# Kernel tuning notes

Hardware: AMD Instinct MI355X
Metric: run time of the kernel (lower is better)

Reference implementation:

```python
import jax, jax.numpy as jnp
import numpy as np

EPS = 1e-5


def _whiten(feature):
    # ZCA whitening per sample (WCT): f_w = U diag(s^-1/2) U^T (f - mean)
    b, c, h, w = feature.shape
    f = feature.reshape(b, c, h * w)
    mean = f.mean(axis=-1, keepdims=True)
    f = f - mean
    cov = jnp.einsum('bcx,bdx->bcd', f, f) / (h * w - 1)
    s, u = jnp.linalg.eigh(cov)
    s = jnp.maximum(s, EPS)
    out = jnp.einsum('bcd,bd,bed,bex->bcx', u, s ** -0.5, u, f)
    return out.reshape(b, c, h, w)


def _color(feature, target):
    # ZCA coloring: f_c = Ut diag(st^1/2) Ut^T (f - mean_f) + mean_t
    b, c, h, w = feature.shape
    f = feature.reshape(b, c, h * w)
    f = f - f.mean(axis=-1, keepdims=True)
    t = target.reshape(b, c, -1)
    tmean = t.mean(axis=-1, keepdims=True)
    tc = t - tmean
    cov = jnp.einsum('bcx,bdx->bcd', tc, tc) / (tc.shape[-1] - 1)
    s, u = jnp.linalg.eigh(cov)
    s = jnp.maximum(s, EPS)
    out = jnp.einsum('bcd,bd,bed,bex->bcx', u, s ** 0.5, u, f) + tmean
    return out.reshape(b, c, h, w)


def _patches(f, p):
    # [b,c,h,w] -> [b,c,h,w,p*p], same ordering as torch unfold(2,p).unfold(3,p)
    pad = (p - 1) // 2
    b, c, h, w = f.shape
    fp = jnp.pad(f, ((0, 0), (0, 0), (pad, pad), (pad, pad)))
    return jnp.stack([fp[:, :, i:i + h, j:j + w] for i in range(p) for j in range(p)], axis=-1)


def reference(content_feature, style_feature, style_strength, patch_size):
    p = int(patch_size)
    pad = (p - 1) // 2
    nc = _whiten(content_feature)
    ns = _whiten(style_feature)
    b, c, h, w = nc.shape
    n = h * w  # one style kernel per style spatial location (stride 1)

    # style kernels [b, n, c, p, p] and their L2 norms over (c,p,p)
    sk = _patches(ns, p).transpose(0, 2, 3, 1, 4).reshape(b, n, c, p, p)
    knorm = jnp.sqrt(jnp.sum(sk ** 2, axis=(2, 3, 4), keepdims=True))
    skn = (sk / knorm).reshape(b, n, c, p * p)

    # patch matching score == conv2d of content with normalized style kernels
    cp = _patches(nc, p)                              # [b,c,h,w,p*p]
    score = jnp.einsum('bchwk,bnck->bnhw', cp, skn)   # [b,n,h,w]

    # argmax one-hot -> gather the best-matching (un-normalized) style patch
    idx = jnp.argmax(score, axis=1)                   # [b,h,w]
    sel = jax.vmap(lambda k, i: k[i])(sk, idx.reshape(b, -1))  # [b,hw,c,p,p]
    sel = sel.reshape(b, h, w, c, p, p).transpose(0, 3, 1, 2, 4, 5)  # [b,c,h,w,p,p]

    # overlap-add == conv_transpose2d(one_hot, kernels, padding=p-1) on padded input
    buf = jnp.zeros((b, c, h + p - 1, w + p - 1), dtype=sel.dtype)
    for di in range(p):
        for dj in range(p):
            buf = buf.at[:, :, di:di + h, dj:dj + w].add(sel[:, :, :, :, di, dj])
    recon = buf[:, :, pad:pad + h, pad:pad + w]

    # overlap counts (norm_deconvolution)
    m = jnp.zeros((h + p - 1, w + p - 1), dtype=sel.dtype)
    for di in range(p):
        for dj in range(p):
            m = m.at[di:di + h, dj:dj + w].add(1.0)
    norm = m[pad:pad + h, pad:pad + w]

    reassembled = recon / norm[None, None]
    stylized = _color(reassembled, style_feature)
    return (1.0 - style_strength) * content_feature + style_strength * stylized


def setup_inputs():
    key = jax.random.key(0)
    k1, k2 = jax.random.split(key)
    B, C, H, W = 2, 256, 48, 48
    return {
        'content_feature': jax.random.normal(k1, (B, C, H, W), jnp.float32),
        'style_feature': jax.random.normal(k2, (B, C, H, W), jnp.float32),
        'style_strength': jnp.float32(1.0),
        'patch_size': 3,
    }
```

## Files before the change

kernel.cpp:

```cpp
#include <hip/hip_runtime.h>

constexpr int B_  = 2;
constexpr int C_  = 256;
constexpr int H_  = 48;
constexpr int W_  = 48;
constexpr int N_  = H_ * W_;
constexpr int PH_ = H_ + 2;
constexpr int PW_ = W_ + 2;
constexpr int NP_ = PH_ * PW_;
constexpr int NPS_ = 2560;
constexpr int MS_  = 2560;
constexpr int CC_ = C_ * C_;
constexpr int NCH_ = 36;
constexpr int NC_  = N_ / NCH_;
constexpr int NSIT_ = 5;
constexpr int KCH_ = 9;

__device__ inline float waveRed(float v) {
  #pragma unroll
  for (int o = 32; o > 0; o >>= 1) v += __shfl_down(v, o);
  return v;
}

#define GEMM64_COMPUTE(sAT, sB, acc, ty, tx)                        \
  _Pragma("unroll")                                                 \
  for (int kk = 0; kk < 16; kk++) {                                 \
    float4 a = *(const float4*)&sAT[kk][(ty) * 4];                  \
    float4 b = *(const float4*)&sB[kk][(tx) * 4];                   \
    acc[0][0] += a.x * b.x; acc[0][1] += a.x * b.y;                 \
    acc[0][2] += a.x * b.z; acc[0][3] += a.x * b.w;                 \
    acc[1][0] += a.y * b.x; acc[1][1] += a.y * b.y;                 \
    acc[1][2] += a.y * b.z; acc[1][3] += a.y * b.w;                 \
    acc[2][0] += a.z * b.x; acc[2][1] += a.z * b.y;                 \
    acc[2][2] += a.z * b.z; acc[2][3] += a.z * b.w;                 \
    acc[3][0] += a.w * b.x; acc[3][1] += a.w * b.y;                 \
    acc[3][2] += a.w * b.z; acc[3][3] += a.w * b.w;                 \
  }


__global__ __launch_bounds__(256) void center_kernel(
    const float* __restrict__ content, const float* __restrict__ style,
    float* __restrict__ fc, float* __restrict__ fs, float* __restrict__ mean_s) {
  int t = blockIdx.x;
  int which = t / (B_ * C_);
  int bc = t % (B_ * C_);
  const float* src = which ? style : content;
  float* dst = which ? fs : fc;
  const float* row = src + (size_t)bc * N_;
  float acc = 0.f;
  for (int i = threadIdx.x; i < N_; i += 256) acc += row[i];
  __shared__ float sm[4];
  float r = waveRed(acc);
  if ((threadIdx.x & 63) == 0) sm[threadIdx.x >> 6] = r;
  __syncthreads();
  float mean = (sm[0] + sm[1] + sm[2] + sm[3]) * (1.0f / N_);
  for (int i = threadIdx.x; i < N_; i += 256) dst[(size_t)bc * N_ + i] = row[i] - mean;
  if (which == 1 && threadIdx.x == 0) mean_s[bc] = mean;
}

__global__ __launch_bounds__(256) void cov_kernel(
    const float* __restrict__ fc, const float* __restrict__ fs, float* __restrict__ pcov) {
  int z = blockIdx.z;
  int m = z & 3, ci = z >> 2;
  const float* f = (m < 2) ? (fc + (size_t)m * C_ * N_) : (fs + (size_t)(m - 2) * C_ * N_);
  int i0 = blockIdx.y * 64, j0 = blockIdx.x * 64;
  int t = threadIdx.x;
  int tx = t & 15, ty = t >> 4;
  int sr = t >> 2, skq = t & 3;
  __shared__ float sAT[16][68], sB[16][68];
  float acc[4][4] = {};
  int k0e = ci * 256 + 256;
  for (int k0 = ci * 256; k0 < k0e; k0 += 16) {
    float4 av = *(const float4*)&f[(size_t)(i0 + sr) * N_ + k0 + skq * 4];
    float4 bv = *(const float4*)&f[(size_t)(j0 + sr) * N_ + k0 + skq * 4];
    __syncthreads();
    sAT[skq * 4 + 0][sr] = av.x; sAT[skq * 4 + 1][sr] = av.y;
    sAT[skq * 4 + 2][sr] = av.z; sAT[skq * 4 + 3][sr] = av.w;
    sB[skq * 4 + 0][sr] = bv.x;  sB[skq * 4 + 1][sr] = bv.y;
    sB[skq * 4 + 2][sr] = bv.z;  sB[skq * 4 + 3][sr] = bv.w;
    __syncthreads();
    GEMM64_COMPUTE(sAT, sB, acc, ty, tx)
  }
  float* out = pcov + ((size_t)ci * 4 + m) * CC_;
  for (int u = 0; u < 4; u++)
    for (int v = 0; v < 4; v++)
      out[(size_t)(i0 + ty * 4 + u) * C_ + (j0 + tx * 4 + v)] = acc[u][v];
}

__global__ __launch_bounds__(256) void covreduce(
    const float* __restrict__ pcov, float* __restrict__ A4) {
  int t = blockIdx.x * 256 + threadIdx.x;
  float acc = 0.f;
  #pragma unroll
  for (int ci = 0; ci < KCH_; ci++) acc += pcov[(size_t)ci * 4 * CC_ + t];
  A4[t] = acc * (1.0f / (float)(N_ - 1));
}

__global__ __launch_bounds__(256) void ns_init(
    const float* __restrict__ A4, float* __restrict__ Yp, float* __restrict__ Zp,
    float* __restrict__ scal) {
  int m = blockIdx.y, s = blockIdx.x;
  const float* A = A4 + (size_t)m * CC_;
  float d = A[(size_t)threadIdx.x * 257];
  __shared__ float sm[4];
  float r = waveRed(d);
  if ((threadIdx.x & 63) == 0) sm[threadIdx.x >> 6] = r;
  __syncthreads();
  float trace = sm[0] + sm[1] + sm[2] + sm[3];
  float sc = 1.1f * trace / (float)C_;
  if (s == 0 && threadIdx.x == 0) scal[m] = sc;
  float inv = 1.0f / sc;
  int i0 = s * (CC_ / 16);
  for (int i = i0 + threadIdx.x; i < i0 + CC_ / 16; i += 256) {
    Yp[(size_t)m * CC_ + i] = A[i] * inv;
    Zp[(size_t)m * CC_ + i] = ((i >> 8) == (i & 255)) ? 1.0f : 0.0f;
    Yp[(size_t)(4 + m) * CC_ + i] = 0.f;
    Zp[(size_t)(4 + m) * CC_ + i] = 0.f;
  }
}

__global__ __launch_bounds__(256) void ns_stepA(
    const float* __restrict__ Zp, const float* __restrict__ Yp, float* __restrict__ Tp) {
  int z = blockIdx.z;
  int m = z & 3, kh = z >> 2;
  const float* A0 = Zp + (size_t)m * CC_;
  const float* A1 = Zp + (size_t)(4 + m) * CC_;
  const float* B0 = Yp + (size_t)m * CC_;
  const float* B1 = Yp + (size_t)(4 + m) * CC_;
  float* out = Tp + (size_t)(kh * 4 + m) * CC_;
  int i0 = blockIdx.y * 32, j0 = blockIdx.x * 32;
  int t = threadIdx.x;
  int tx = t & 15, ty = t >> 4;
  int sr = t >> 3, sc4 = t & 7;
  __shared__ float sAT[32][36], sB[32][36];
  float acc[2][2] = {};
  int k0e = kh * 128 + 128;
  for (int k0 = kh * 128; k0 < k0e; k0 += 32) {
    size_t ia = (size_t)(i0 + sr) * 256 + k0 + sc4 * 4;
    size_t ib = (size_t)(k0 + sr) * 256 + j0 + sc4 * 4;
    float4 a0 = *(const float4*)&A0[ia];
    float4 a1 = *(const float4*)&A1[ia];
    float4 b0 = *(const float4*)&B0[ib];
    float4 b1 = *(const float4*)&B1[ib];
    float4 av = {a0.x + a1.x, a0.y + a1.y, a0.z + a1.z, a0.w + a1.w};
    float4 bv = {b0.x + b1.x, b0.y + b1.y, b0.z + b1.z, b0.w + b1.w};
    __syncthreads();
    sAT[sc4 * 4 + 0][sr] = av.x; sAT[sc4 * 4 + 1][sr] = av.y;
    sAT[sc4 * 4 + 2][sr] = av.z; sAT[sc4 * 4 + 3][sr] = av.w;
    *(float4*)&sB[sr][sc4 * 4] = bv;
    __syncthreads();
    #pragma unroll
    for (int kk = 0; kk < 32; kk++) {
      float2 a = *(const float2*)&sAT[kk][ty * 2];
      float2 b = *(const float2*)&sB[kk][tx * 2];
      acc[0][0] += a.x * b.x; acc[0][1] += a.x * b.y;
      acc[1][0] += a.y * b.x; acc[1][1] += a.y * b.y;
    }
    __syncthreads();
  }
  for (int u = 0; u < 2; u++)
    for (int v = 0; v < 2; v++) {
      int i = i0 + ty * 2 + u, j = j0 + tx * 2 + v;
      float d = (kh == 0 && i == j) ? 3.0f : 0.0f;
      out[(size_t)i * 256 + j] = d - acc[u][v];
    }
}

__global__ __launch_bounds__(256) void ns_stepB(
    const float* __restrict__ Yp, const float* __restrict__ Zp, const float* __restrict__ Tp,
    float* __restrict__ Ynp, float* __restrict__ Znp) {
  int z = blockIdx.z;
  int m = z & 3, kh = (z >> 2) & 1;
  bool doY = (z < 8);
  const float* A0 = (doY ? Yp : Tp) + (size_t)m * CC_;
  const float* A1 = (doY ? Yp : Tp) + (size_t)(4 + m) * CC_;
  const float* B0 = (doY ? Tp : Zp) + (size_t)m * CC_;
  const float* B1 = (doY ? Tp : Zp) + (size_t)(4 + m) * CC_;
  float* out = (doY ? Ynp : Znp) + (size_t)(kh * 4 + m) * CC_;
  int i0 = blockIdx.y * 32, j0 = blockIdx.x * 32;
  int t = threadIdx.x;
  int tx = t & 15, ty = t >> 4;
  int sr = t >> 3, sc4 = t & 7;
  __shared__ float sAT[32][36], sB[32][36];
  float acc[2][2] = {};
  int k0e = kh * 128 + 128;
  for (int k0 = kh * 128; k0 < k0e; k0 += 32) {
    size_t ia = (size_t)(i0 + sr) * 256 + k0 + sc4 * 4;
    size_t ib = (size_t)(k0 + sr) * 256 + j0 + sc4 * 4;
    float4 a0 = *(const float4*)&A0[ia];
    float4 a1 = *(const float4*)&A1[ia];
    float4 b0 = *(const float4*)&B0[ib];
    float4 b1 = *(const float4*)&B1[ib];
    float4 av = {a0.x + a1.x, a0.y + a1.y, a0.z + a1.z, a0.w + a1.w};
    float4 bv = {b0.x + b1.x, b0.y + b1.y, b0.z + b1.z, b0.w + b1.w};
    __syncthreads();
    sAT[sc4 * 4 + 0][sr] = av.x; sAT[sc4 * 4 + 1][sr] = av.y;
    sAT[sc4 * 4 + 2][sr] = av.z; sAT[sc4 * 4 + 3][sr] = av.w;
    *(float4*)&sB[sr][sc4 * 4] = bv;
    __syncthreads();
    #pragma unroll
    for (int kk = 0; kk < 32; kk++) {
      float2 a = *(const float2*)&sAT[kk][ty * 2];
      float2 b = *(const float2*)&sB[kk][tx * 2];
      acc[0][0] += a.x * b.x; acc[0][1] += a.x * b.y;
      acc[1][0] += a.y * b.x; acc[1][1] += a.y * b.y;
    }
    __syncthreads();
  }
  for (int u = 0; u < 2; u++)
    for (int v = 0; v < 2; v++) {
      int i = i0 + ty * 2 + u, j = j0 + tx * 2 + v;
      out[(size_t)i * 256 + j] = 0.5f * acc[u][v];
    }
}

__global__ __launch_bounds__(256) void whiten_pad(
    const float* __restrict__ Zf, const float* __restrict__ scal,
    const float* __restrict__ fc, const float* __restrict__ fs,
    float* __restrict__ ncP, float* __restrict__ nsP, float* __restrict__ nsT) {
  int m = blockIdx.z;
  const float* f = (m < 2) ? (fc + (size_t)m * C_ * N_) : (fs + (size_t)(m - 2) * C_ * N_);
  int c0 = blockIdx.y * 64, x0 = blockIdx.x * 64;
  int t = threadIdx.x;
  int tx = t & 15, ty = t >> 4;
  int sr = t >> 2, skq = t & 3;
  int bkk = t & 15, bc4 = t >> 4;
  __shared__ float sAT[16][68], sB[16][68];
  float acc[4][4] = {};
  for (int k0 = 0; k0 < 256; k0 += 16) {
    size_t ia = (size_t)(c0 + sr) * 256 + k0 + skq * 4;
    float4 a0 = *(const float4*)&Zf[(size_t)m * CC_ + ia];
    float4 a1 = *(const float4*)&Zf[(size_t)(4 + m) * CC_ + ia];
    float4 av = {a0.x + a1.x, a0.y + a1.y, a0.z + a1.z, a0.w + a1.w};
    float4 bv = *(const float4*)&f[(size_t)(k0 + bkk) * N_ + x0 + bc4 * 4];
    __syncthreads();
    sAT[skq * 4 + 0][sr] = av.x; sAT[skq * 4 + 1][sr] = av.y;
    sAT[skq * 4 + 2][sr] = av.z; sAT[skq * 4 + 3][sr] = av.w;
    *(float4*)&sB[bkk][bc4 * 4] = bv;
    __syncthreads();
    GEMM64_COMPUTE(sAT, sB, acc, ty, tx)
  }
  float rs = rsqrtf(scal[m]);
  int b = (m < 2) ? m : (m - 2);
  for (int u = 0; u < 4; u++)
    for (int v = 0; v < 4; v++) {
      int c = c0 + ty * 4 + u, x = x0 + tx * 4 + v;
      int h = x / W_, w = x % W_;
      int pp = (h + 1) * PW_ + (w + 1);
      float val = acc[u][v] * rs;
      if (m < 2) {
        ncP[((size_t)b * C_ + c) * NPS_ + pp] = val;
      } else {
        nsP[((size_t)b * NP_ + pp) * C_ + c] = val;
        nsT[((size_t)b * C_ + c) * NPS_ + pp] = val;
      }
    }
}

__global__ __launch_bounds__(256) void q_kernel(const float* __restrict__ nsP, float* __restrict__ q) {
  int wid = (blockIdx.x * 256 + threadIdx.x) >> 6;
  int lane = threadIdx.x & 63;
  if (wid >= B_ * NP_) return;
  const float* v = nsP + (size_t)wid * C_;
  float acc = 0.f;
  #pragma unroll
  for (int c = lane; c < C_; c += 64) { float t = v[c]; acc += t * t; }
  acc = waveRed(acc);
  if (lane == 0) q[wid] = acc;
}

__global__ __launch_bounds__(256) void kninv_kernel(const float* __restrict__ q, float* __restrict__ kninv) {
  int t = blockIdx.x * 256 + threadIdx.x;
  if (t >= B_ * N_) return;
  int b = t / N_, n = t % N_;
  int hn = n / W_, wn = n % W_;
  const float* qb = q + (size_t)b * NP_ + hn * PW_ + wn;
  float s = 0.f;
  #pragma unroll
  for (int i = 0; i < 3; i++)
    #pragma unroll
    for (int j = 0; j < 3; j++) s += qb[i * PW_ + j];
  kninv[t] = rsqrtf(s);
}

__global__ __launch_bounds__(256) void m_kernel(
    const float* __restrict__ At, const float* __restrict__ Bt, float* __restrict__ M,
    size_t batchA, size_t batchM) {
  size_t bz = blockIdx.z;
  At += bz * batchA; Bt += bz * batchA; M += bz * batchM;
  int i0 = blockIdx.y * 64, j0 = blockIdx.x * 128;
  int t = threadIdx.x;
  int tx = t & 15, ty = t >> 4;
  int akk = t >> 4, ac4 = t & 15;
  int bkk = t >> 5, bc4 = t & 31;
  __shared__ float sA[16][68], sB[16][132];
  float acc[4][8] = {};
  for (int k0 = 0; k0 < 256; k0 += 16) {
    float4 a0 = *(const float4*)&At[(size_t)(k0 + akk) * NPS_ + i0 + ac4 * 4];
    float4 b0 = *(const float4*)&Bt[(size_t)(k0 + bkk) * NPS_ + j0 + bc4 * 4];
    float4 b1 = *(const float4*)&Bt[(size_t)(k0 + bkk + 8) * NPS_ + j0 + bc4 * 4];
    __syncthreads();
    *(float4*)&sA[akk][ac4 * 4] = a0;
    *(float4*)&sB[bkk][bc4 * 4] = b0;
    *(float4*)&sB[bkk + 8][bc4 * 4] = b1;
    __syncthreads();
    #pragma unroll
    for (int kk = 0; kk < 16; kk++) {
      float4 a  = *(const float4*)&sA[kk][ty * 4];
      float4 p  = *(const float4*)&sB[kk][tx * 4];
      float4 qv = *(const float4*)&sB[kk][64 + tx * 4];
      acc[0][0] += a.x * p.x; acc[0][1] += a.x * p.y; acc[0][2] += a.x * p.z; acc[0][3] += a.x * p.w;
      acc[1][0] += a.y * p.x; acc[1][1] += a.y * p.y; acc[1][2] += a.y * p.z; acc[1][3] += a.y * p.w;
      acc[2][0] += a.z * p.x; acc[2][1] += a.z * p.y; acc[2][2] += a.z * p.z; acc[2][3] += a.z * p.w;
      acc[3][0] += a.w * p.x; acc[3][1] += a.w * p.y; acc[3][2] += a.w * p.z; acc[3][3] += a.w * p.w;
      acc[0][4] += a.x * qv.x; acc[0][5] += a.x * qv.y; acc[0][6] += a.x * qv.z; acc[0][7] += a.x * qv.w;
      acc[1][4] += a.y * qv.x; acc[1][5] += a.y * qv.y; acc[1][6] += a.y * qv.z; acc[1][7] += a.y * qv.w;
      acc[2][4] += a.z * qv.x; acc[2][5] += a.z * qv.y; acc[2][6] += a.z * qv.z; acc[2][7] += a.z * qv.w;
      acc[3][4] += a.w * qv.x; acc[3][5] += a.w * qv.y; acc[3][6] += a.w * qv.z; acc[3][7] += a.w * qv.w;
    }
    __syncthreads();
  }
  #pragma unroll
  for (int u = 0; u < 4; u++) {
    size_t row = (size_t)(i0 + ty * 4 + u) * MS_;
    float4 s0 = {acc[u][0], acc[u][1], acc[u][2], acc[u][3]};
    float4 s1 = {acc[u][4], acc[u][5], acc[u][6], acc[u][7]};
    *(float4*)&M[row + j0 + tx * 4] = s0;
    *(float4*)&M[row + j0 + 64 + tx * 4] = s1;
  }
}

__global__ __launch_bounds__(256) void score_kernel(
    const float* __restrict__ M, const float* __restrict__ kninv,
    float* __restrict__ pval, int* __restrict__ pidx, int b0, size_t batchM) {
  int b = b0 + blockIdx.z;
  M += (size_t)blockIdx.z * batchM;
  int m = blockIdx.x * 256 + threadIdx.x;
  int h = m / W_, w = m % W_;
  int cm = h * PW_ + w;
  int n0 = blockIdx.y * NC_;
  const float* kni = kninv + (size_t)b * N_;
  float best = -3.4e38f;
  int bidx = n0;
  for (int n = n0; n < n0 + NC_; n++) {
    int hn = n / W_, wn = n % W_;
    int rn = hn * PW_ + wn;
    const float* base = M + (size_t)rn * MS_ + cm;
    float s = 0.f;
    #pragma unroll
    for (int i = 0; i < 3; i++)
      #pragma unroll
      for (int j = 0; j < 3; j++) s += base[(size_t)(i * PW_ + j) * (MS_ + 1)];
    s *= kni[n];
    if (s > best) { best = s; bidx = n; }
  }
  pval[((size_t)b * NCH_ + blockIdx.y) * N_ + m] = best;
  pidx[((size_t)b * NCH_ + blockIdx.y) * N_ + m] = bidx;
}

__global__ __launch_bounds__(256) void argmax_final(
    const float* __restrict__ pval, const int* __restrict__ pidx, int* __restrict__ idxb) {
  int t = blockIdx.x * 256 + threadIdx.x;
  if (t >= B_ * N_) return;
  int b = t / N_, m = t % N_;
  float best = -3.4e38f; int bidx = 0;
  for (int ch = 0; ch < NCH_; ch++) {
    float v = pval[((size_t)b * NCH_ + ch) * N_ + m];
    int i = pidx[((size_t)b * NCH_ + ch) * N_ + m];
    if (v > best) { best = v; bidx = i; }
  }
  idxb[t] = bidx;
}

__global__ __launch_bounds__(256) void reassemble_kernel(
    const float* __restrict__ nsP, const int* __restrict__ idxb, float* __restrict__ recon) {
  int bm = blockIdx.x;
  int b = bm / N_, m = bm % N_;
  int h = m / W_, w = m % W_;
  int c = threadIdx.x;
  float acc = 0.f; int cnt = 0;
  for (int di = 0; di < 3; di++) {
    int hs = h + 1 - di; if (hs < 0 || hs >= H_) continue;
    for (int dj = 0; dj < 3; dj++) {
      int ws = w + 1 - dj; if (ws < 0 || ws >= W_) continue;
      int n = idxb[(size_t)b * N_ + hs * W_ + ws];
      int hn = n / W_, wn = n % W_;
      int pp = (hn + di) * PW_ + (wn + dj);
      acc += nsP[((size_t)b * NP_ + pp) * C_ + c];
      cnt++;
    }
  }
  recon[((size_t)b * N_ + m) * C_ + c] = acc / (float)cnt;
}

__global__ __launch_bounds__(256) void rmean_part(const float* __restrict__ recon, float* __restrict__ pmr) {
  int b = blockIdx.y, ch = blockIdx.x, c = threadIdx.x;
  float acc = 0.f;
  int x0 = ch * (N_ / 16);
  for (int x = x0; x < x0 + (N_ / 16); x++) acc += recon[((size_t)b * N_ + x) * C_ + c];
  pmr[((size_t)b * 16 + ch) * C_ + c] = acc;
}

__global__ __launch_bounds__(256) void rmean_fin(const float* __restrict__ pmr, float* __restrict__ mr) {
  int b = blockIdx.x, c = threadIdx.x;
  float acc = 0.f;
  for (int ch = 0; ch < 16; ch++) acc += pmr[((size_t)b * 16 + ch) * C_ + c];
  mr[(size_t)b * C_ + c] = acc * (1.0f / N_);
}

__global__ __launch_bounds__(256) void color_blend(
    const float* __restrict__ Yf, const float* __restrict__ scal,
    const float* __restrict__ recon, const float* __restrict__ mr,
    const float* __restrict__ msty, const float* __restrict__ content,
    const float* __restrict__ ssp, float* __restrict__ out) {
  int b = blockIdx.z;
  int m = 2 + b;
  int c0 = blockIdx.y * 64, x0 = blockIdx.x * 64;
  int t = threadIdx.x;
  int tx = t & 15, ty = t >> 4;
  int sr = t >> 2, skq = t & 3;
  __shared__ float sAT[16][68], sB[16][68];
  float acc[4][4] = {};
  for (int k0 = 0; k0 < 256; k0 += 16) {
    size_t ia = (size_t)(c0 + sr) * 256 + k0 + skq * 4;
    float4 a0 = *(const float4*)&Yf[(size_t)m * CC_ + ia];
    float4 a1 = *(const float4*)&Yf[(size_t)(4 + m) * CC_ + ia];
    float4 av = {a0.x + a1.x, a0.y + a1.y, a0.z + a1.z, a0.w + a1.w};
    float4 bm4 = *(const float4*)&mr[(size_t)b * C_ + k0 + skq * 4];
    float4 bv = *(const float4*)&recon[((size_t)b * N_ + x0 + sr) * C_ + k0 + skq * 4];
    bv.x -= bm4.x; bv.y -= bm4.y; bv.z -= bm4.z; bv.w -= bm4.w;
    __syncthreads();
    sAT[skq * 4 + 0][sr] = av.x; sAT[skq * 4 + 1][sr] = av.y;
    sAT[skq * 4 + 2][sr] = av.z; sAT[skq * 4 + 3][sr] = av.w;
    sB[skq * 4 + 0][sr] = bv.x;  sB[skq * 4 + 1][sr] = bv.y;
    sB[skq * 4 + 2][sr] = bv.z;  sB[skq * 4 + 3][sr] = bv.w;
    __syncthreads();
    GEMM64_COMPUTE(sAT, sB, acc, ty, tx)
  }
  float sq = sqrtf(scal[m]);
  float ss = ssp[0];
  for (int u = 0; u < 4; u++)
    for (int v = 0; v < 4; v++) {
      int c = c0 + ty * 4 + u, x = x0 + tx * 4 + v;
      float sty = acc[u][v] * sq + msty[(size_t)b * C_ + c];
      size_t o = ((size_t)b * C_ + c) * N_ + x;
      out[o] = (1.0f - ss) * content[o] + ss * sty;
    }
}

extern "C" void kernel_launch(void* const* d_in, const int* in_sizes, int n_in,
                              void* d_out, int out_size, void* d_ws, size_t ws_size,
                              hipStream_t stream) {
  (void)in_sizes; (void)n_in; (void)out_size;
  const float* content = (const float*)d_in[0];
  const float* style   = (const float*)d_in[1];
  const float* ssp     = (const float*)d_in[2];
  float* out = (float*)d_out;
  float* W = (float*)d_ws;

  size_t off = 0;
  float* fc   = W + off; off += (size_t)B_ * C_ * N_;
  float* fs   = W + off; off += (size_t)B_ * C_ * N_;
  float* nsP  = W + off; off += (size_t)B_ * NP_ * C_;
  float* nsT  = W + off; off += (size_t)B_ * C_ * NPS_;
  float* ncP  = W + off; off += (size_t)B_ * C_ * NPS_;
  float* A4   = W + off; off += (size_t)4 * CC_;
  float* Ya   = W + off; off += (size_t)8 * CC_;
  float* Yb   = W + off; off += (size_t)8 * CC_;
  float* Za   = W + off; off += (size_t)8 * CC_;
  float* Zb   = W + off; off += (size_t)8 * CC_;
  float* scal = W + off; off += 4;
  float* msty = W + off; off += (size_t)B_ * C_;
  float* mr   = W + off; off += (size_t)B_ * C_;
  float* pmr  = W + off; off += (size_t)B_ * 16 * C_;
  float* q    = W + off; off += (size_t)B_ * NP_;
  float* kni  = W + off; off += (size_t)B_ * N_;
  float* pval = W + off; off += (size_t)B_ * NCH_ * N_;
  float* Mb   = W + off;
  size_t off_Mb = off;

  size_t off1 = off_Mb + (size_t)MS_ * MS_;
  size_t off2 = off_Mb + (size_t)2 * MS_ * MS_;
  size_t tail = (size_t)B_ * NCH_ * N_ + (size_t)B_ * N_;
  bool dual = ws_size >= (off2 + tail) * sizeof(float);
  size_t offM = dual ? off2 : off1;
  int* pidx = (int*)(W + offM);
  int* idxb = (int*)(W + offM + (size_t)B_ * NCH_ * N_);
  float* pcov = Mb;
  float* T    = Mb;
  float* recon = fs;

  hipMemsetAsync(nsP, 0, (size_t)B_ * NP_ * C_ * sizeof(float), stream);
  hipMemsetAsync(nsT, 0, (size_t)B_ * C_ * NPS_ * sizeof(float), stream);
  hipMemsetAsync(ncP, 0, (size_t)B_ * C_ * NPS_ * sizeof(float), stream);

  center_kernel<<<2 * B_ * C_, 256, 0, stream>>>(content, style, fc, fs, msty);
  cov_kernel<<<dim3(4, 4, 4 * KCH_), 256, 0, stream>>>(fc, fs, pcov);
  covreduce<<<4 * CC_ / 256, 256, 0, stream>>>(pcov, A4);
  ns_init<<<dim3(16, 4), 256, 0, stream>>>(A4, Ya, Za, scal);

  float *Ycur = Ya, *Zcur = Za, *Yalt = Yb, *Zalt = Zb;
  for (int it = 0; it < NSIT_; it++) {
    ns_stepA<<<dim3(8, 8, 8), 256, 0, stream>>>(Zcur, Ycur, T);
    ns_stepB<<<dim3(8, 8, 16), 256, 0, stream>>>(Ycur, Zcur, T, Yalt, Zalt);
    float* tp;
    tp = Ycur; Ycur = Yalt; Yalt = tp;
    tp = Zcur; Zcur = Zalt; Zalt = tp;
  }

  whiten_pad<<<dim3(36, 4, 4), 256, 0, stream>>>(Zcur, scal, fc, fs, ncP, nsP, nsT);
  q_kernel<<<(B_ * NP_ + 3) / 4, 256, 0, stream>>>(nsP, q);
  kninv_kernel<<<(B_ * N_ + 255) / 256, 256, 0, stream>>>(q, kni);

  if (dual) {
    m_kernel<<<dim3(20, 40, 2), 256, 0, stream>>>(
        nsT, ncP, Mb, (size_t)C_ * NPS_, (size_t)MS_ * MS_);
    score_kernel<<<dim3(N_ / 256, NCH_, 2), 256, 0, stream>>>(
        Mb, kni, pval, pidx, 0, (size_t)MS_ * MS_);
  } else {
    for (int b = 0; b < B_; b++) {
      m_kernel<<<dim3(20, 40, 1), 256, 0, stream>>>(
          nsT + (size_t)b * C_ * NPS_, ncP + (size_t)b * C_ * NPS_, Mb, 0, 0);
      score_kernel<<<dim3(N_ / 256, NCH_, 1), 256, 0, stream>>>(
          Mb, kni, pval, pidx, b, 0);
    }
  }
  argmax_final<<<(B_ * N_ + 255) / 256, 256, 0, stream>>>(pval, pidx, idxb);
  reassemble_kernel<<<B_ * N_, 256, 0, stream>>>(nsP, idxb, recon);
  rmean_part<<<dim3(16, B_), 256, 0, stream>>>(recon, pmr);
  rmean_fin<<<B_, 256, 0, stream>>>(pmr, mr);
  color_blend<<<dim3(36, 4, B_), 256, 0, stream>>>(
      Ycur, scal, recon, mr, msty, content, ssp, out);
}
```

Baseline: 362.5 us.

## Exploit symmetry in covariance and Newton-Schulz GEMMs; deepen m_kernel K tile; double score chunks

Covariance and Newton-Schulz products are symmetric, so only lower-triangular tiles are computed and each result is mirrored to the transposed position. This roughly halves the GEMM blocks in those kernels. Separately, the m_kernel K-tile grows from 16 to 32 to halve the number of barriers per block, and the score chunk count NCH_ doubles from 36 to 72 for more parallelism in the argmax reduction. The symmetry trick relies on Y, Z and T staying symmetric in Newton-Schulz, which holds mathematically but only approximately in floating point; the mirrored writes are also uncoalesced.

```diff
diff --git a/kernel.cpp b/kernel.cpp
--- a/kernel.cpp
+++ b/kernel.cpp
@@ -11,7 +11,7 @@
 constexpr int NPS_ = 2560;
 constexpr int MS_  = 2560;
 constexpr int CC_ = C_ * C_;
-constexpr int NCH_ = 36;
+constexpr int NCH_ = 72;
 constexpr int NC_  = N_ / NCH_;
 constexpr int NSIT_ = 5;
 constexpr int KCH_ = 9;
@@ -20,6 +20,12 @@
   #pragma unroll
   for (int o = 32; o > 0; o >>= 1) v += __shfl_down(v, o);
   return v;
+}
+
+__device__ inline void triDecode(int u, int& ti, int& tj) {
+  int t = 0;
+  while ((t + 1) * (t + 2) / 2 <= u) t++;
+  ti = t; tj = u - t * (t + 1) / 2;
 }
 
 #define GEMM64_COMPUTE(sAT, sB, acc, ty, tx)                        \
@@ -63,7 +69,8 @@
   int z = blockIdx.z;
   int m = z & 3, ci = z >> 2;
   const float* f = (m < 2) ? (fc + (size_t)m * C_ * N_) : (fs + (size_t)(m - 2) * C_ * N_);
-  int i0 = blockIdx.y * 64, j0 = blockIdx.x * 64;
+  int ti, tj; triDecode(blockIdx.x, ti, tj);
+  int i0 = ti * 64, j0 = tj * 64;
   int t = threadIdx.x;
   int tx = t & 15, ty = t >> 4;
   int sr = t >> 2, skq = t & 3;
@@ -83,8 +90,11 @@
   }
   float* out = pcov + ((size_t)ci * 4 + m) * CC_;
   for (int u = 0; u < 4; u++)
-    for (int v = 0; v < 4; v++)
-      out[(size_t)(i0 + ty * 4 + u) * C_ + (j0 + tx * 4 + v)] = acc[u][v];
+    for (int v = 0; v < 4; v++) {
+      int i = i0 + ty * 4 + u, j = j0 + tx * 4 + v;
+      out[(size_t)i * C_ + j] = acc[u][v];
+      if (ti != tj) out[(size_t)j * C_ + i] = acc[u][v];
+    }
 }
 
 __global__ __launch_bounds__(256) void covreduce(
@@ -128,7 +138,8 @@
   const float* B0 = Yp + (size_t)m * CC_;
   const float* B1 = Yp + (size_t)(4 + m) * CC_;
   float* out = Tp + (size_t)(kh * 4 + m) * CC_;
-  int i0 = blockIdx.y * 32, j0 = blockIdx.x * 32;
+  int ti, tj; triDecode(blockIdx.x, ti, tj);
+  int i0 = ti * 32, j0 = tj * 32;
   int t = threadIdx.x;
   int tx = t & 15, ty = t >> 4;
   int sr = t >> 3, sc4 = t & 7;
@@ -162,7 +173,9 @@
     for (int v = 0; v < 2; v++) {
       int i = i0 + ty * 2 + u, j = j0 + tx * 2 + v;
       float d = (kh == 0 && i == j) ? 3.0f : 0.0f;
-      out[(size_t)i * 256 + j] = d - acc[u][v];
+      float val = d - acc[u][v];
+      out[(size_t)i * 256 + j] = val;
+      if (ti != tj) out[(size_t)j * 256 + i] = val;
     }
 }
 
@@ -177,7 +190,8 @@
   const float* B0 = (doY ? Tp : Zp) + (size_t)m * CC_;
   const float* B1 = (doY ? Tp : Zp) + (size_t)(4 + m) * CC_;
   float* out = (doY ? Ynp : Znp) + (size_t)(kh * 4 + m) * CC_;
-  int i0 = blockIdx.y * 32, j0 = blockIdx.x * 32;
+  int ti, tj; triDecode(blockIdx.x, ti, tj);
+  int i0 = ti * 32, j0 = tj * 32;
   int t = threadIdx.x;
   int tx = t & 15, ty = t >> 4;
   int sr = t >> 3, sc4 = t & 7;
@@ -210,7 +224,9 @@
   for (int u = 0; u < 2; u++)
     for (int v = 0; v < 2; v++) {
       int i = i0 + ty * 2 + u, j = j0 + tx * 2 + v;
-      out[(size_t)i * 256 + j] = 0.5f * acc[u][v];
+      float val = 0.5f * acc[u][v];
+      out[(size_t)i * 256 + j] = val;
+      if (ti != tj) out[(size_t)j * 256 + i] = val;
     }
 }
 
@@ -291,21 +307,27 @@
   int i0 = blockIdx.y * 64, j0 = blockIdx.x * 128;
   int t = threadIdx.x;
   int tx = t & 15, ty = t >> 4;
-  int akk = t >> 4, ac4 = t & 15;
-  int bkk = t >> 5, bc4 = t & 31;
-  __shared__ float sA[16][68], sB[16][132];
+  int ak = t >> 4, ac = t & 15;
+  int bk = t >> 5, bc = t & 31;
+  __shared__ float sA[32][68], sB[32][132];
   float acc[4][8] = {};
-  for (int k0 = 0; k0 < 256; k0 += 16) {
-    float4 a0 = *(const float4*)&At[(size_t)(k0 + akk) * NPS_ + i0 + ac4 * 4];
-    float4 b0 = *(const float4*)&Bt[(size_t)(k0 + bkk) * NPS_ + j0 + bc4 * 4];
-    float4 b1 = *(const float4*)&Bt[(size_t)(k0 + bkk + 8) * NPS_ + j0 + bc4 * 4];
-    __syncthreads();
-    *(float4*)&sA[akk][ac4 * 4] = a0;
-    *(float4*)&sB[bkk][bc4 * 4] = b0;
-    *(float4*)&sB[bkk + 8][bc4 * 4] = b1;
+  for (int k0 = 0; k0 < 256; k0 += 32) {
+    float4 a0 = *(const float4*)&At[(size_t)(k0 + ak) * NPS_ + i0 + ac * 4];
+    float4 a1 = *(const float4*)&At[(size_t)(k0 + ak + 16) * NPS_ + i0 + ac * 4];
+    float4 b0 = *(const float4*)&Bt[(size_t)(k0 + bk) * NPS_ + j0 + bc * 4];
+    float4 b1 = *(const float4*)&Bt[(size_t)(k0 + bk + 8) * NPS_ + j0 + bc * 4];
+    float4 b2 = *(const float4*)&Bt[(size_t)(k0 + bk + 16) * NPS_ + j0 + bc * 4];
+    float4 b3 = *(const float4*)&Bt[(size_t)(k0 + bk + 24) * NPS_ + j0 + bc * 4];
+    __syncthreads();
+    *(float4*)&sA[ak][ac * 4] = a0;
+    *(float4*)&sA[ak + 16][ac * 4] = a1;
+    *(float4*)&sB[bk][bc * 4] = b0;
+    *(float4*)&sB[bk + 8][bc * 4] = b1;
+    *(float4*)&sB[bk + 16][bc * 4] = b2;
+    *(float4*)&sB[bk + 24][bc * 4] = b3;
     __syncthreads();
     #pragma unroll
-    for (int kk = 0; kk < 16; kk++) {
+    for (int kk = 0; kk < 32; kk++) {
       float4 a  = *(const float4*)&sA[kk][ty * 4];
       float4 p  = *(const float4*)&sB[kk][tx * 4];
       float4 qv = *(const float4*)&sB[kk][64 + tx * 4];
@@ -495,14 +517,14 @@
   hipMemsetAsync(ncP, 0, (size_t)B_ * C_ * NPS_ * sizeof(float), stream);
 
   center_kernel<<<2 * B_ * C_, 256, 0, stream>>>(content, style, fc, fs, msty);
-  cov_kernel<<<dim3(4, 4, 4 * KCH_), 256, 0, stream>>>(fc, fs, pcov);
+  cov_kernel<<<dim3(10, 1, 4 * KCH_), 256, 0, stream>>>(fc, fs, pcov);
   covreduce<<<4 * CC_ / 256, 256, 0, stream>>>(pcov, A4);
   ns_init<<<dim3(16, 4), 256, 0, stream>>>(A4, Ya, Za, scal);
 
   float *Ycur = Ya, *Zcur = Za, *Yalt = Yb, *Zalt = Zb;
   for (int it = 0; it < NSIT_; it++) {
-    ns_stepA<<<dim3(8, 8, 8), 256, 0, stream>>>(Zcur, Ycur, T);
-    ns_stepB<<<dim3(8, 8, 16), 256, 0, stream>>>(Ycur, Zcur, T, Yalt, Zalt);
+    ns_stepA<<<dim3(36, 1, 8), 256, 0, stream>>>(Zcur, Ycur, T);
+    ns_stepB<<<dim3(36, 1, 16), 256, 0, stream>>>(Ycur, Zcur, T, Yalt, Zalt);
     float* tp;
     tp = Ycur; Ycur = Yalt; Yalt = tp;
     tp = Zcur; Zcur = Zalt; Zalt = tp;
```

Result: slower. 374.8 us (+3.4%).
